# Optimization experiments

Measured on AMD Instinct MI355X. Metric: run time of the kernel, lower is better.

The kernel has to match this reference:

```python
import jax, jax.numpy as jnp
import numpy as np

CUTOFF = 1.5   # cutoff_val from __init__
M = 48         # atoms per molecule (batch_node_vec is block-structured: node n belongs to molecule n // M)
B = 128        # number of molecules


def setup_inputs() -> dict:
    key = jax.random.key(0)
    k1, k2 = jax.random.split(key)
    N = B * M
    coords = jax.random.normal(k1, (N, 3), dtype=jnp.float32)
    atomic_ns = jax.random.randint(k2, (N,), 0, 10)
    batch_node_vec = jnp.arange(N, dtype=jnp.int64) // M
    return {"atomic_ns": atomic_ns, "coords": coords, "batch_node_vec": batch_node_vec}


def _forward(coords):
    # coords: [N, 3]; molecules are contiguous blocks of M atoms -> dense per-molecule blocks.
    N = coords.shape[0]
    c = coords.reshape(N // M, M, 3)                      # [B, M, 3]
    diff = c[:, :, None, :] - c[:, None, :, :]            # diff[b,p,q] = r_p - r_q, [B,M,M,3]
    d2 = jnp.sum(diff * diff, axis=-1)                    # squared pair distances [B,M,M]
    offdiag = ~jnp.eye(M, dtype=bool)
    dist = jnp.sqrt(jnp.where(offdiag, d2, 1.0))          # safe sqrt (diagonal masked out)
    adj = offdiag & (dist < CUTOFF)                       # radius graph within each molecule
    dists = jnp.where(adj, dist, 0.0)                     # per-edge distances (masked dense form)

    # Triplets k->j->i (DimeNet): angle at center j between (r_i - r_j) and (r_k - r_j), i != k.
    v = jnp.swapaxes(diff, 1, 2)                          # v[b,j,i] = r_i - r_j, [B,M,M,3]
    a = jnp.einsum('bjid,bjkd->bjik', v, v)               # dot products [B,M,M,M]
    n2 = d2                                               # |v[b,j,i]|^2 (d2 is symmetric)
    # |u x w|^2 = |u|^2 |w|^2 - (u.w)^2  (same value as torch.cross(...).norm()**2)
    b2 = jnp.maximum(n2[:, :, :, None] * n2[:, :, None, :] - a * a, 0.0)
    tmask = adj[:, :, :, None] & adj[:, :, None, :] & offdiag[None, None, :, :]  # edges (j,i),(j,k), i!=k
    b_safe = jnp.sqrt(jnp.where(tmask & (b2 > 0), b2, 1.0))
    b_val = jnp.where(b2 > 0, b_safe, 0.0)
    a_safe = jnp.where(tmask, a, 1.0)
    ang = jnp.arctan2(b_val, a_safe)
    angles = jnp.where(tmask, ang, 0.0)                   # [B,M,M,M] masked triplet angles
    return dists, angles


def reference(atomic_ns, coords, batch_node_vec):
    # atomic_ns / batch_node_vec only determine graph structure (ints); geometry uses coords.
    return _forward(coords)
```

## Files before the change

kernel.cpp:

```cpp
#include <hip/hip_runtime.h>

#define MM 48
#define BMOL 128
#define CUTOFF_V 1.5f
#define PI_F 3.14159265358979f

typedef float v4f __attribute__((ext_vector_type(4)));

__global__ __launch_bounds__(576)
void dimenet_dist_angle_kernel(const float* __restrict__ coords,
                               float* __restrict__ dists,
                               float* __restrict__ angles)
{
    const int bj = blockIdx.x;
    const int b  = bj / MM;
    const int j  = bj - b * MM;

    __shared__ __align__(16) float sx[MM];
    __shared__ __align__(16) float sy[MM];
    __shared__ __align__(16) float sz[MM];
    __shared__ __align__(16) float sw[MM];

    const int t = threadIdx.x;

    if (t < MM) {
        const float* cj = coords + 3 * ((size_t)b * MM + j);
        const float* ci = coords + 3 * ((size_t)b * MM + t);
        float dx = ci[0] - cj[0];
        float dy = ci[1] - cj[1];
        float dz = ci[2] - cj[2];
        float d2 = dx * dx + dy * dy + dz * dz;
        float dist = sqrtf(d2);
        bool adj = (t != j) && (dist < CUTOFF_V);
        sx[t] = dx;
        sy[t] = dy;
        sz[t] = dz;
        sw[t] = adj ? rsqrtf(d2) : 0.0f;
        __builtin_nontemporal_store(adj ? dist : 0.0f,
                                    dists + ((size_t)b * MM + j) * MM + t);
    }
    __syncthreads();

    const int i  = t / 12;
    const int k0 = (t - i * 12) * 4;

    const float xi = sx[i], yi = sy[i], zi = sz[i], wi = sw[i];
    const float4 xk = *(const float4*)&sx[k0];
    const float4 yk = *(const float4*)&sy[k0];
    const float4 zk = *(const float4*)&sz[k0];
    const float4 wk = *(const float4*)&sw[k0];

    const float* pxk = &xk.x;
    const float* pyk = &yk.x;
    const float* pzk = &zk.x;
    const float* pwk = &wk.x;

    float ang[4];
#pragma unroll
    for (int e = 0; e < 4; ++e) {
        float a = xi * pxk[e] + yi * pyk[e] + zi * pzk[e];
        float w = wi * pwk[e];
        float x = a * w;
        x = fminf(fmaxf(x, -1.0f), 1.0f);
        float s = fabsf(x);
        float p = sqrtf(1.0f - s) *
                  (1.5707288f + s * (-0.2121144f + s * (0.074261f - 0.0187293f * s)));
        float r = (x >= 0.0f) ? p : (PI_F - p);
        bool mask = (w > 0.0f) && (i != k0 + e);
        ang[e] = mask ? r : 0.0f;
    }

    v4f res = {ang[0], ang[1], ang[2], ang[3]};
    __builtin_nontemporal_store(
        res, (v4f*)(angles + (((size_t)b * MM + j) * MM + i) * MM + k0));
}

extern "C" void kernel_launch(void* const* d_in, const int* in_sizes, int n_in,
                              void* d_out, int out_size, void* d_ws, size_t ws_size,
                              hipStream_t stream) {
    const float* coords = (const float*)d_in[1];

    float* out    = (float*)d_out;
    float* dists  = out;
    float* angles = out + (size_t)BMOL * MM * MM;

    dim3 grid(BMOL * MM);
    dim3 block(576);
    dimenet_dist_angle_kernel<<<grid, block, 0, stream>>>(coords, dists, angles);
}
```

Before: 20.45 us.

## Split into separate dists and angles kernels with grid-stride recomputation

```diff
diff --git a/kernel.cpp b/kernel.cpp
--- a/kernel.cpp
+++ b/kernel.cpp
@@ -7,72 +7,99 @@
 
 typedef float v4f __attribute__((ext_vector_type(4)));
 
-__global__ __launch_bounds__(576)
-void dimenet_dist_angle_kernel(const float* __restrict__ coords,
-                               float* __restrict__ dists,
-                               float* __restrict__ angles)
+__device__ __forceinline__ float acos_poly(float x) {
+    x = fminf(fmaxf(x, -1.0f), 1.0f);
+    float s = fabsf(x);
+    float p = sqrtf(1.0f - s) *
+              (1.5707288f + s * (-0.2121144f + s * (0.074261f - 0.0187293f * s)));
+    return (x >= 0.0f) ? p : (PI_F - p);
+}
+
+#define ANG_BLOCKS 1728
+#define ANG_ITERS  8
+__global__ __launch_bounds__(256)
+void angles_kernel(const float* __restrict__ coords,
+                   float* __restrict__ angles)
 {
-    const int bj = blockIdx.x;
-    const int b  = bj / MM;
-    const int j  = bj - b * MM;
+    const int tid = blockIdx.x * 256 + threadIdx.x;
+    const int nthreads = ANG_BLOCKS * 256;
 
-    __shared__ __align__(16) float sx[MM];
-    __shared__ __align__(16) float sy[MM];
-    __shared__ __align__(16) float sz[MM];
-    __shared__ __align__(16) float sw[MM];
+#pragma unroll
+    for (int it = 0; it < ANG_ITERS; ++it) {
+        int q = tid + it * nthreads;
+        int q12 = q / 12;
+        int k0  = (q - q12 * 12) * 4;
+        int i   = q12 % 48;
+        int t2  = q12 / 48;
+        int j   = t2 % 48;
+        int b   = t2 / 48;
 
-    const int t = threadIdx.x;
+        const float* cb = coords + (size_t)b * (MM * 3);
+        float jx = cb[j * 3], jy = cb[j * 3 + 1], jz = cb[j * 3 + 2];
+        float ix = cb[i * 3], iy = cb[i * 3 + 1], iz = cb[i * 3 + 2];
+        v4f c0 = *(const v4f*)(cb + k0 * 3);
+        v4f c1 = *(const v4f*)(cb + k0 * 3 + 4);
+        v4f c2 = *(const v4f*)(cb + k0 * 3 + 8);
+        float kc[12] = {c0.x, c0.y, c0.z, c0.w, c1.x, c1.y, c1.z, c1.w,
+                        c2.x, c2.y, c2.z, c2.w};
 
-    if (t < MM) {
-        const float* cj = coords + 3 * ((size_t)b * MM + j);
-        const float* ci = coords + 3 * ((size_t)b * MM + t);
-        float dx = ci[0] - cj[0];
-        float dy = ci[1] - cj[1];
-        float dz = ci[2] - cj[2];
-        float d2 = dx * dx + dy * dy + dz * dz;
-        float dist = sqrtf(d2);
-        bool adj = (t != j) && (dist < CUTOFF_V);
-        sx[t] = dx;
-        sy[t] = dy;
-        sz[t] = dz;
-        sw[t] = adj ? rsqrtf(d2) : 0.0f;
-        __builtin_nontemporal_store(adj ? dist : 0.0f,
-                                    dists + ((size_t)b * MM + j) * MM + t);
+        float vix = ix - jx, viy = iy - jy, viz = iz - jz;
+        float n2i = vix * vix + viy * viy + viz * viz;
+        bool adji = (i != j) && (sqrtf(n2i) < CUTOFF_V);
+        float wi  = adji ? rsqrtf(n2i) : 0.0f;
+
+        float ang[4];
+#pragma unroll
+        for (int e = 0; e < 4; ++e) {
+            float vkx = kc[3 * e]     - jx;
+            float vky = kc[3 * e + 1] - jy;
+            float vkz = kc[3 * e + 2] - jz;
+            float n2k = vkx * vkx + vky * vky + vkz * vkz;
+            int   k   = k0 + e;
+            bool adjk = (k != j) && (sqrtf(n2k) < CUTOFF_V);
+            float wk  = adjk ? rsqrtf(n2k) : 0.0f;
+            float a   = vix * vkx + viy * vky + viz * vkz;
+            float w   = wi * wk;
+            float r   = acos_poly(a * w);
+            bool mask = (w > 0.0f) && (i != k);
+            ang[e] = mask ? r : 0.0f;
+        }
+
+        v4f res = {ang[0], ang[1], ang[2], ang[3]};
+        __builtin_nontemporal_store(res, (v4f*)(angles + (size_t)q * 4));
     }
-    __syncthreads();
+}
 
-    const int i  = t / 12;
-    const int k0 = (t - i * 12) * 4;
+__global__ __launch_bounds__(256)
+void dists_kernel(const float* __restrict__ coords,
+                  float* __restrict__ dists)
+{
+    const int q = blockIdx.x * 256 + threadIdx.x;
+    int rem = q % 576;
+    int b   = q / 576;
+    int j   = rem / 12;
+    int k0  = (rem - j * 12) * 4;
 
-    const float xi = sx[i], yi = sy[i], zi = sz[i], wi = sw[i];
-    const float4 xk = *(const float4*)&sx[k0];
-    const float4 yk = *(const float4*)&sy[k0];
-    const float4 zk = *(const float4*)&sz[k0];
-    const float4 wk = *(const float4*)&sw[k0];
+    const float* cb = coords + (size_t)b * (MM * 3);
+    float jx = cb[j * 3], jy = cb[j * 3 + 1], jz = cb[j * 3 + 2];
+    v4f c0 = *(const v4f*)(cb + k0 * 3);
+    v4f c1 = *(const v4f*)(cb + k0 * 3 + 4);
+    v4f c2 = *(const v4f*)(cb + k0 * 3 + 8);
+    float kc[12] = {c0.x, c0.y, c0.z, c0.w, c1.x, c1.y, c1.z, c1.w,
+                    c2.x, c2.y, c2.z, c2.w};
 
-    const float* pxk = &xk.x;
-    const float* pyk = &yk.x;
-    const float* pzk = &zk.x;
-    const float* pwk = &wk.x;
-
-    float ang[4];
+    float d[4];
 #pragma unroll
     for (int e = 0; e < 4; ++e) {
-        float a = xi * pxk[e] + yi * pyk[e] + zi * pzk[e];
-        float w = wi * pwk[e];
-        float x = a * w;
-        x = fminf(fmaxf(x, -1.0f), 1.0f);
-        float s = fabsf(x);
-        float p = sqrtf(1.0f - s) *
-                  (1.5707288f + s * (-0.2121144f + s * (0.074261f - 0.0187293f * s)));
-        float r = (x >= 0.0f) ? p : (PI_F - p);
-        bool mask = (w > 0.0f) && (i != k0 + e);
-        ang[e] = mask ? r : 0.0f;
+        float dx = kc[3 * e]     - jx;
+        float dy = kc[3 * e + 1] - jy;
+        float dz = kc[3 * e + 2] - jz;
+        float dist = sqrtf(dx * dx + dy * dy + dz * dz);
+        bool adj = ((k0 + e) != j) && (dist < CUTOFF_V);
+        d[e] = adj ? dist : 0.0f;
     }
-
-    v4f res = {ang[0], ang[1], ang[2], ang[3]};
-    __builtin_nontemporal_store(
-        res, (v4f*)(angles + (((size_t)b * MM + j) * MM + i) * MM + k0));
+    v4f res = {d[0], d[1], d[2], d[3]};
+    __builtin_nontemporal_store(res, (v4f*)(dists + (size_t)q * 4));
 }
 
 extern "C" void kernel_launch(void* const* d_in, const int* in_sizes, int n_in,
@@ -84,7 +111,6 @@
     float* dists  = out;
     float* angles = out + (size_t)BMOL * MM * MM;
 
-    dim3 grid(BMOL * MM);
-    dim3 block(576);
-    dimenet_dist_angle_kernel<<<grid, block, 0, stream>>>(coords, dists, angles);
+    dists_kernel<<<dim3(288), dim3(256), 0, stream>>>(coords, dists);
+    angles_kernel<<<dim3(ANG_BLOCKS), dim3(256), 0, stream>>>(coords, angles);
 }
```

Result: slower. 40.27 us (+96.9%).

## Use single-wavefront blocks looping over the angle slice with padded shared layout

Applied to the files above, without the earlier changes.

```diff
diff --git a/kernel.cpp b/kernel.cpp
--- a/kernel.cpp
+++ b/kernel.cpp
@@ -7,72 +7,77 @@
 
 typedef float v4f __attribute__((ext_vector_type(4)));
 
-__global__ __launch_bounds__(576)
-void dimenet_dist_angle_kernel(const float* __restrict__ coords,
-                               float* __restrict__ dists,
-                               float* __restrict__ angles)
+__device__ __forceinline__ float acos_poly(float x) {
+    x = fminf(fmaxf(x, -1.0f), 1.0f);
+    float s = fabsf(x);
+    float p = sqrtf(1.0f - s) *
+              (1.5707288f + s * (-0.2121144f + s * (0.074261f - 0.0187293f * s)));
+    return (x >= 0.0f) ? p : (PI_F - p);
+}
+
+__global__ __launch_bounds__(64, 6)
+void slice_kernel(const float* __restrict__ coords,
+                  float* __restrict__ dists,
+                  float* __restrict__ angles)
 {
     const int bj = blockIdx.x;
     const int b  = bj / MM;
     const int j  = bj - b * MM;
 
-    __shared__ __align__(16) float sx[MM];
-    __shared__ __align__(16) float sy[MM];
-    __shared__ __align__(16) float sz[MM];
-    __shared__ __align__(16) float sw[MM];
+    __shared__ __align__(16) float paos[MM * 8];
+    __shared__ __align__(16) float sxp[240];
+    __shared__ __align__(16) float syp[240];
+    __shared__ __align__(16) float szp[240];
+    __shared__ __align__(16) float swp[240];
 
     const int t = threadIdx.x;
 
     if (t < MM) {
-        const float* cj = coords + 3 * ((size_t)b * MM + j);
-        const float* ci = coords + 3 * ((size_t)b * MM + t);
-        float dx = ci[0] - cj[0];
-        float dy = ci[1] - cj[1];
-        float dz = ci[2] - cj[2];
+        const float* cb = coords + b * (MM * 3);
+        const float jx = cb[j * 3], jy = cb[j * 3 + 1], jz = cb[j * 3 + 2];
+        float dx = cb[t * 3]     - jx;
+        float dy = cb[t * 3 + 1] - jy;
+        float dz = cb[t * 3 + 2] - jz;
         float d2 = dx * dx + dy * dy + dz * dz;
         float dist = sqrtf(d2);
         bool adj = (t != j) && (dist < CUTOFF_V);
-        sx[t] = dx;
-        sy[t] = dy;
-        sz[t] = dz;
-        sw[t] = adj ? rsqrtf(d2) : 0.0f;
+        float w  = adj ? rsqrtf(d2) : 0.0f;
+        *(v4f*)&paos[t * 8] = (v4f){dx, dy, dz, w};
+        int widx = 20 * (t >> 2) + (t & 3);
+        sxp[widx] = dx; syp[widx] = dy; szp[widx] = dz; swp[widx] = w;
         __builtin_nontemporal_store(adj ? dist : 0.0f,
-                                    dists + ((size_t)b * MM + j) * MM + t);
+                                    dists + (size_t)bj * MM + t);
     }
     __syncthreads();
 
-    const int i  = t / 12;
-    const int k0 = (t - i * 12) * 4;
+    float* ang_base = angles + (size_t)bj * (MM * MM);
 
-    const float xi = sx[i], yi = sy[i], zi = sz[i], wi = sw[i];
-    const float4 xk = *(const float4*)&sx[k0];
-    const float4 yk = *(const float4*)&sy[k0];
-    const float4 zk = *(const float4*)&sz[k0];
-    const float4 wk = *(const float4*)&sw[k0];
+#pragma unroll 3
+    for (int it = 0; it < 9; ++it) {
+        const int q = t + it * 64;
+        const int i = q / 12;
+        const int m = q - i * 12;
+        const int k0 = m * 4;
 
-    const float* pxk = &xk.x;
-    const float* pyk = &yk.x;
-    const float* pzk = &zk.x;
-    const float* pwk = &wk.x;
+        v4f pi = *(const v4f*)&paos[i * 8];
+        v4f xk = *(const v4f*)&sxp[m * 20];
+        v4f yk = *(const v4f*)&syp[m * 20];
+        v4f zk = *(const v4f*)&szp[m * 20];
+        v4f wk = *(const v4f*)&swp[m * 20];
 
-    float ang[4];
+        float ang[4];
 #pragma unroll
-    for (int e = 0; e < 4; ++e) {
-        float a = xi * pxk[e] + yi * pyk[e] + zi * pzk[e];
-        float w = wi * pwk[e];
-        float x = a * w;
-        x = fminf(fmaxf(x, -1.0f), 1.0f);
-        float s = fabsf(x);
-        float p = sqrtf(1.0f - s) *
-                  (1.5707288f + s * (-0.2121144f + s * (0.074261f - 0.0187293f * s)));
-        float r = (x >= 0.0f) ? p : (PI_F - p);
-        bool mask = (w > 0.0f) && (i != k0 + e);
-        ang[e] = mask ? r : 0.0f;
+        for (int e = 0; e < 4; ++e) {
+            float a  = pi.x * xk[e] + pi.y * yk[e] + pi.z * zk[e];
+            float wp = pi.w * wk[e];
+            float r  = acos_poly(a * wp);
+            bool mask = (wp > 0.0f) && (i != k0 + e);
+            ang[e] = mask ? r : 0.0f;
+        }
+
+        __builtin_nontemporal_store((v4f){ang[0], ang[1], ang[2], ang[3]},
+                                    (v4f*)(ang_base + q * 4));
     }
-
-    v4f res = {ang[0], ang[1], ang[2], ang[3]};
-    __builtin_nontemporal_store(
-        res, (v4f*)(angles + (((size_t)b * MM + j) * MM + i) * MM + k0));
 }
 
 extern "C" void kernel_launch(void* const* d_in, const int* in_sizes, int n_in,
@@ -84,7 +89,5 @@
     float* dists  = out;
     float* angles = out + (size_t)BMOL * MM * MM;
 
-    dim3 grid(BMOL * MM);
-    dim3 block(576);
-    dimenet_dist_angle_kernel<<<grid, block, 0, stream>>>(coords, dists, angles);
+    slice_kernel<<<dim3(BMOL * MM), dim3(64), 0, stream>>>(coords, dists, angles);
 }
```

After: 21.34 us. 1.04x slower.
